# Kernel optimization log

Hardware: AMD Instinct MI355X
Metric: run time of the kernel (lower is better)

The kernel has to match this reference:

```python
import jax, jax.numpy as jnp
import numpy as np

N = 50000        # nodes
E = 1_600_000    # edges (avg degree 32)
IN = 8           # in_channels
OUT = 64         # out_channels / hidden
K = 2            # Chebyshev order


def setup_inputs() -> dict:
    key = jax.random.key(0)
    ks = jax.random.split(key, 16)
    w = lambda k, s: (jax.random.normal(k, s, jnp.float32) * 0.05)
    inp = {
        "x": jax.random.normal(ks[0], (N, IN), jnp.float32),
        "H": jax.random.normal(ks[1], (N, OUT), jnp.float32),
        "edge_index": jax.random.randint(ks[2], (2, E), 0, N, dtype=jnp.int64),
    }
    names = [("z_x", IN), ("z_h", OUT), ("r_x", IN), ("r_h", OUT), ("c_x", IN), ("c_h", OUT)]
    for i, (nm, d) in enumerate(names):
        inp["W_" + nm] = w(ks[3 + 2 * i], (K, d, OUT))
        inp["b_" + nm] = w(ks[4 + 2 * i], (OUT,))
    return inp


def _cheb(x, W, b, row, col, norm):
    # PyG-style ChebConv with lambda_max=2: L_hat = -D^{-1/2} A D^{-1/2}
    # Tx0 = x; Tx1 = L_hat x; Tx_k = 2 L_hat Tx_{k-1} - Tx_{k-2}
    out = x @ W[0]
    Tx0 = x
    Tx1 = jax.ops.segment_sum(norm[:, None] * x[col], row, num_segments=N)
    out = out + Tx1 @ W[1]
    for k in range(2, W.shape[0]):
        Tx2 = 2.0 * jax.ops.segment_sum(norm[:, None] * Tx1[col], row, num_segments=N) - Tx0
        out = out + Tx2 @ W[k]
        Tx0, Tx1 = Tx1, Tx2
    return out + b


def reference(x, H, edge_index, W_z_x, b_z_x, W_z_h, b_z_h, W_r_x, b_r_x,
              W_r_h, b_r_h, W_c_x, b_c_x, W_c_h, b_c_h):
    row, col = edge_index[0], edge_index[1]
    deg = jax.ops.segment_sum(jnp.ones((E,), x.dtype), row, num_segments=N)
    dinv = jnp.where(deg > 0, 1.0 / jnp.sqrt(jnp.where(deg > 0, deg, 1.0)), 0.0)
    norm = -dinv[row] * dinv[col]  # sym-normalized, negated adjacency (L - I)

    Z = jax.nn.sigmoid(_cheb(x, W_z_x, b_z_x, row, col, norm)
                       + _cheb(H, W_z_h, b_z_h, row, col, norm))
    R = jax.nn.sigmoid(_cheb(x, W_r_x, b_r_x, row, col, norm)
                       + _cheb(H, W_r_h, b_r_h, row, col, norm))
    C = jnp.tanh(_cheb(x, W_c_x, b_c_x, row, col, norm)
                 + _cheb(R * H, W_c_h, b_c_h, row, col, norm))
    return Z * H + (1.0 - Z) * C
```

## Files before the change

### kernel.cpp

```cpp
#include <hip/hip_runtime.h>
#include <hip/hip_fp16.h>
#include <math.h>

#define IN_CH 8
#define OUT_CH 64
#define NPW 8

__device__ __forceinline__ unsigned short f2h(float f) {
    return __half_as_ushort(__float2half_rn(f));
}
__device__ __forceinline__ float h2f_lo(unsigned v) {
    return __half2float(__ushort_as_half((unsigned short)(v & 0xFFFFu)));
}
__device__ __forceinline__ float h2f_hi(unsigned v) {
    return __half2float(__ushort_as_half((unsigned short)(v >> 16)));
}
__device__ __forceinline__ float sigmoidf(float v) { return 1.0f / (1.0f + expf(-v)); }

__global__ void deg_kernel(const int* __restrict__ row, int* __restrict__ deg, int E) {
    int i = blockIdx.x * blockDim.x + threadIdx.x;
    if (i < E) atomicAdd(&deg[row[i]], 1);
}

__global__ void dinv_kernel(const int* __restrict__ deg, float* __restrict__ dinv, int N) {
    int i = blockIdx.x * blockDim.x + threadIdx.x;
    if (i < N) {
        int d = deg[i];
        dinv[i] = (d > 0) ? rsqrtf((float)d) : 0.f;
    }
}

__global__ void scan_kernel(const int* __restrict__ deg, int* __restrict__ rowptr,
                            int* __restrict__ cursor, int N) {
    __shared__ int s_wave[17];
    __shared__ int s_running;
    int tid = threadIdx.x;
    int lane = tid & 63, wid = tid >> 6;
    if (tid == 0) s_running = 0;
    __syncthreads();
    for (int base = 0; base < N; base += 1024) {
        int i = base + tid;
        int v = (i < N) ? deg[i] : 0;
        int incl = v;
#pragma unroll
        for (int off = 1; off < 64; off <<= 1) {
            int t = __shfl_up(incl, off, 64);
            if (lane >= off) incl += t;
        }
        if (lane == 63) s_wave[wid] = incl;
        __syncthreads();
        if (wid == 0) {
            int wv = (lane < 16) ? s_wave[lane] : 0;
            int winc = wv;
#pragma unroll
            for (int off = 1; off < 16; off <<= 1) {
                int t = __shfl_up(winc, off, 64);
                if (lane >= off) winc += t;
            }
            if (lane < 16) s_wave[lane] = winc - wv;
            if (lane == 15) s_wave[16] = winc;
        }
        __syncthreads();
        int run = s_running;
        int excl = run + s_wave[wid] + incl - v;
        if (i < N) { rowptr[i] = excl; cursor[i] = excl; }
        __syncthreads();
        if (tid == 0) s_running = run + s_wave[16];
        __syncthreads();
    }
    if (tid == 0) rowptr[N] = s_running;
}

__global__ void bucket_kernel(const int* __restrict__ ei, int* __restrict__ cursor,
                              int* __restrict__ col_s, int E) {
    int e = blockIdx.x * blockDim.x + threadIdx.x;
    if (e >= E) return;
    int r = ei[e];
    int c = ei[E + e];
    int pos = atomicAdd(&cursor[r], 1);
    col_s[pos] = c;
}

__global__ void xform_kernel(const float* __restrict__ src, unsigned short* __restrict__ dst,
                             const float* __restrict__ dinv, int total4, int logd) {
    int i = blockIdx.x * blockDim.x + threadIdx.x;
    if (i >= total4) return;
    int el = i * 4;
    float s = dinv[el >> logd];
    float4 v = reinterpret_cast<const float4*>(src)[i];
    ushort4 o;
    o.x = f2h(v.x * s); o.y = f2h(v.y * s); o.z = f2h(v.z * s); o.w = f2h(v.w * s);
    reinterpret_cast<ushort4*>(dst)[i] = o;
}

__global__ void zrow_kernel(unsigned short* xb, unsigned short* Hb, unsigned short* RHb, int N) {
    int t = threadIdx.x;
    if (t < IN_CH) xb[(size_t)N * IN_CH + t] = 0;
    Hb[(size_t)N * OUT_CH + t] = 0;
    RHb[(size_t)N * OUT_CH + t] = 0;
}

__global__ void g64_kernel(const int* __restrict__ rowptr, const int* __restrict__ col_s,
                           const float* __restrict__ dinv, const unsigned short* __restrict__ srcb,
                           float* __restrict__ dst, int N) {
    int n = blockIdx.x * (blockDim.x >> 6) + (threadIdx.x >> 6);
    int lane = threadIdx.x & 63;
    int half = lane >> 5;
    int sl = lane & 31;
    if (n >= N) return;
    int beg = rowptr[n], end = rowptr[n + 1];
    const unsigned* src32 = reinterpret_cast<const unsigned*>(srcb);
    float a0 = 0.f, a1 = 0.f;
    for (int base = beg; base < end; base += 64) {
        int cnt = min(end - base, 64);
        int mycol = col_s[base + min(lane, cnt - 1)];
#pragma unroll 4
        for (int e = 0; e < cnt; e += 2) {
            int idx = e + half;
            int c = __shfl(mycol, idx, 64);
            c = (idx < cnt) ? c : N;
            unsigned v = src32[(c << 5) + sl];
            a0 += h2f_lo(v);
            a1 += h2f_hi(v);
        }
    }
    a0 += __shfl_xor(a0, 32, 64);
    a1 += __shfl_xor(a1, 32, 64);
    if (half == 0) {
        float s = -dinv[n];
        reinterpret_cast<float2*>(dst)[(size_t)n * 32 + sl] = make_float2(s * a0, s * a1);
    }
}

__global__ void g8_kernel(const int* __restrict__ rowptr, const int* __restrict__ col_s,
                          const float* __restrict__ dinv, const unsigned short* __restrict__ srcb,
                          float* __restrict__ dst, int N) {
    int n = blockIdx.x * (blockDim.x >> 6) + (threadIdx.x >> 6);
    int lane = threadIdx.x & 63;
    int g = lane >> 2;
    int o2 = lane & 3;
    if (n >= N) return;
    int beg = rowptr[n], end = rowptr[n + 1];
    const unsigned* src32 = reinterpret_cast<const unsigned*>(srcb);
    float a0 = 0.f, a1 = 0.f;
    for (int j = beg + g; j < end; j += 16) {
        int c = col_s[j];
        unsigned v = src32[(c << 2) + o2];
        a0 += h2f_lo(v);
        a1 += h2f_hi(v);
    }
#pragma unroll
    for (int m = 4; m < 64; m <<= 1) {
        a0 += __shfl_xor(a0, m, 64);
        a1 += __shfl_xor(a1, m, 64);
    }
    if (lane < 4) {
        float s = -dinv[n];
        reinterpret_cast<float2*>(dst)[(size_t)n * 4 + o2] = make_float2(s * a0, s * a1);
    }
}

__global__ __launch_bounds__(256) void gates_kernel(
        const float* __restrict__ x, const float* __restrict__ H,
        const float* __restrict__ Lx, const float* __restrict__ LH,
        const float* __restrict__ dinv,
        const float* __restrict__ Wzx, const float* __restrict__ bzx,
        const float* __restrict__ Wzh, const float* __restrict__ bzh,
        const float* __restrict__ Wrx, const float* __restrict__ brx,
        const float* __restrict__ Wrh, const float* __restrict__ brh,
        float* __restrict__ Z, float* __restrict__ RH, unsigned short* __restrict__ RHb, int N) {
    int wid = threadIdx.x >> 6;
    int lane = threadIdx.x & 63;
    int n0 = blockIdx.x * (4 * NPW) + wid * NPW;

    float axl[NPW], hreg[NPW], lhreg[NPW], accZ[NPW], accR[NPW], dv[NPW];
    float bz = bzx[lane] + bzh[lane];
    float br = brx[lane] + brh[lane];
#pragma unroll
    for (int i = 0; i < NPW; ++i) {
        int nn = min(n0 + i, N - 1);
        axl[i]   = (lane < 8) ? x[(size_t)nn * IN_CH + lane]
                 : (lane < 16 ? Lx[(size_t)nn * IN_CH + (lane - 8)] : 0.f);
        hreg[i]  = H[(size_t)nn * OUT_CH + lane];
        lhreg[i] = LH[(size_t)nn * OUT_CH + lane];
        dv[i]    = dinv[nn];
        accZ[i] = bz;
        accR[i] = br;
    }
#pragma unroll
    for (int k = 0; k < IN_CH; ++k) {
        float wz0 = Wzx[k * 64 + lane], wz1 = Wzx[512 + k * 64 + lane];
        float wr0 = Wrx[k * 64 + lane], wr1 = Wrx[512 + k * 64 + lane];
#pragma unroll
        for (int i = 0; i < NPW; ++i) {
            float xv  = __shfl(axl[i], k, 64);
            float lxv = __shfl(axl[i], k + 8, 64);
            accZ[i] = fmaf(xv, wz0, fmaf(lxv, wz1, accZ[i]));
            accR[i] = fmaf(xv, wr0, fmaf(lxv, wr1, accR[i]));
        }
    }
#pragma unroll 4
    for (int k = 0; k < OUT_CH; ++k) {
        float wh0 = Wzh[k * 64 + lane], wh1 = Wzh[4096 + k * 64 + lane];
        float wr0 = Wrh[k * 64 + lane], wr1 = Wrh[4096 + k * 64 + lane];
#pragma unroll
        for (int i = 0; i < NPW; ++i) {
            float hv  = __shfl(hreg[i], k, 64);
            float lhv = __shfl(lhreg[i], k, 64);
            accZ[i] = fmaf(hv, wh0, fmaf(lhv, wh1, accZ[i]));
            accR[i] = fmaf(hv, wr0, fmaf(lhv, wr1, accR[i]));
        }
    }
#pragma unroll
    for (int i = 0; i < NPW; ++i) {
        int n = n0 + i;
        if (n < N) {
            float z = sigmoidf(accZ[i]);
            float r = sigmoidf(accR[i]);
            float rh = r * hreg[i];
            Z[(size_t)n * OUT_CH + lane]  = z;
            RH[(size_t)n * OUT_CH + lane] = rh;
            RHb[(size_t)n * OUT_CH + lane] = f2h(dv[i] * rh);
        }
    }
}

__global__ __launch_bounds__(256) void final_kernel(
        const float* __restrict__ x, const float* __restrict__ H,
        const float* __restrict__ Lx, const float* __restrict__ RH,
        const float* __restrict__ LRH,
        const float* __restrict__ Wcx, const float* __restrict__ bcx,
        const float* __restrict__ Wch, const float* __restrict__ bch,
        const float* __restrict__ Z, float* __restrict__ out, int N) {
    int wid = threadIdx.x >> 6;
    int lane = threadIdx.x & 63;
    int n0 = blockIdx.x * (4 * NPW) + wid * NPW;

    float axl[NPW], rhreg[NPW], lrhreg[NPW], accC[NPW];
    float bc = bcx[lane] + bch[lane];
#pragma unroll
    for (int i = 0; i < NPW; ++i) {
        int nn = min(n0 + i, N - 1);
        axl[i]    = (lane < 8) ? x[(size_t)nn * IN_CH + lane]
                  : (lane < 16 ? Lx[(size_t)nn * IN_CH + (lane - 8)] : 0.f);
        rhreg[i]  = RH[(size_t)nn * OUT_CH + lane];
        lrhreg[i] = LRH[(size_t)nn * OUT_CH + lane];
        accC[i] = bc;
    }
#pragma unroll
    for (int k = 0; k < IN_CH; ++k) {
        float wc0 = Wcx[k * 64 + lane], wc1 = Wcx[512 + k * 64 + lane];
#pragma unroll
        for (int i = 0; i < NPW; ++i) {
            float xv  = __shfl(axl[i], k, 64);
            float lxv = __shfl(axl[i], k + 8, 64);
            accC[i] = fmaf(xv, wc0, fmaf(lxv, wc1, accC[i]));
        }
    }
#pragma unroll 4
    for (int k = 0; k < OUT_CH; ++k) {
        float wh0 = Wch[k * 64 + lane], wh1 = Wch[4096 + k * 64 + lane];
#pragma unroll
        for (int i = 0; i < NPW; ++i) {
            float rv  = __shfl(rhreg[i], k, 64);
            float lrv = __shfl(lrhreg[i], k, 64);
            accC[i] = fmaf(rv, wh0, fmaf(lrv, wh1, accC[i]));
        }
    }
#pragma unroll
    for (int i = 0; i < NPW; ++i) {
        int n = n0 + i;
        if (n < N) {
            float c = tanhf(accC[i]);
            float z = Z[(size_t)n * OUT_CH + lane];
            float h = H[(size_t)n * OUT_CH + lane];
            out[(size_t)n * OUT_CH + lane] = z * h + (1.0f - z) * c;
        }
    }
}

extern "C" void kernel_launch(void* const* d_in, const int* in_sizes, int n_in,
                              void* d_out, int out_size, void* d_ws, size_t ws_size,
                              hipStream_t stream) {
    const float* x   = (const float*)d_in[0];
    const float* H   = (const float*)d_in[1];
    const int*   ei  = (const int*)d_in[2];
    const float* Wzx = (const float*)d_in[3];
    const float* bzx = (const float*)d_in[4];
    const float* Wzh = (const float*)d_in[5];
    const float* bzh = (const float*)d_in[6];
    const float* Wrx = (const float*)d_in[7];
    const float* brx = (const float*)d_in[8];
    const float* Wrh = (const float*)d_in[9];
    const float* brh = (const float*)d_in[10];
    const float* Wcx = (const float*)d_in[11];
    const float* bcx = (const float*)d_in[12];
    const float* Wch = (const float*)d_in[13];
    const float* bch = (const float*)d_in[14];

    const int N = in_sizes[0] / IN_CH;
    const int E = in_sizes[2] / 2;

    int*   deg    = (int*)d_ws;
    float* dinv   = (float*)(deg + N);
    int*   rowptr = (int*)(dinv + N);
    int*   col_s  = rowptr + (N + 2);
    unsigned short* xb  = (unsigned short*)(col_s + E);
    unsigned short* Hb  = xb + (size_t)(N + 1) * IN_CH;
    unsigned short* RHb = Hb + (size_t)(N + 1) * OUT_CH;
    float* Lx  = (float*)(RHb + (size_t)(N + 1) * OUT_CH);
    float* LH  = Lx + (size_t)N * IN_CH;
    float* Z   = LH + (size_t)N * OUT_CH;
    float* RH  = Z  + (size_t)N * OUT_CH;
    float* LRH = LH;
    int*   cursor = deg;

    hipMemsetAsync(deg, 0, (size_t)N * sizeof(int), stream);

    const int tb = 256;
    deg_kernel<<<(E + tb - 1) / tb, tb, 0, stream>>>(ei, deg, E);
    dinv_kernel<<<(N + tb - 1) / tb, tb, 0, stream>>>(deg, dinv, N);
    scan_kernel<<<1, 1024, 0, stream>>>(deg, rowptr, cursor, N);
    bucket_kernel<<<(E + tb - 1) / tb, tb, 0, stream>>>(ei, cursor, col_s, E);

    {
        int t4 = N * OUT_CH / 4;
        xform_kernel<<<(t4 + tb - 1) / tb, tb, 0, stream>>>(H, Hb, dinv, t4, 6);
        t4 = N * IN_CH / 4;
        xform_kernel<<<(t4 + tb - 1) / tb, tb, 0, stream>>>(x, xb, dinv, t4, 3);
        zrow_kernel<<<1, 64, 0, stream>>>(xb, Hb, RHb, N);
    }

    const int nblk4 = (N + 3) / 4;
    const int nblkD = (N + 4 * NPW - 1) / (4 * NPW);

    g8_kernel <<<nblk4, tb, 0, stream>>>(rowptr, col_s, dinv, xb, Lx, N);
    g64_kernel<<<nblk4, tb, 0, stream>>>(rowptr, col_s, dinv, Hb, LH, N);

    gates_kernel<<<nblkD, tb, 0, stream>>>(x, H, Lx, LH, dinv, Wzx, bzx, Wzh, bzh,
                                           Wrx, brx, Wrh, brh, Z, RH, RHb, N);

    g64_kernel<<<nblk4, tb, 0, stream>>>(rowptr, col_s, dinv, RHb, LRH, N);

    final_kernel<<<nblkD, tb, 0, stream>>>(x, H, Lx, RH, LRH, Wcx, bcx, Wch, bch,
                                           Z, (float*)d_out, N);
}
```

Baseline: 661.4 us.

## Partition degree and bucket atomics by row range across block groups

Degree counting and CSR bucketing are split into 8 row-range partitions. Blocks are assigned by blockIdx mod 8, and each block scans all edges but only does atomics for rows in its own range. The intent is to localize atomic traffic (likely to an XCD/L2 slice on MI355X) so contention and cross-die coherence cost go down. In exchange, the edge row array is read 8 times.

Result: faster. 612.3 us (-7.4%).

```diff
diff --git a/kernel.cpp b/kernel.cpp
--- a/kernel.cpp
+++ b/kernel.cpp
@@ -17,9 +17,16 @@
 }
 __device__ __forceinline__ float sigmoidf(float v) { return 1.0f / (1.0f + expf(-v)); }
 
-__global__ void deg_kernel(const int* __restrict__ row, int* __restrict__ deg, int E) {
-    int i = blockIdx.x * blockDim.x + threadIdx.x;
-    if (i < E) atomicAdd(&deg[row[i]], 1);
+__global__ void degP_kernel(const int* __restrict__ row, int* __restrict__ deg,
+                            int E, int RPP) {
+    int p = blockIdx.x & 7;
+    int sub = blockIdx.x >> 3;
+    int nsub = gridDim.x >> 3;
+    int lo = p * RPP, hi = lo + RPP;
+    for (int e = sub * blockDim.x + threadIdx.x; e < E; e += nsub * blockDim.x) {
+        int r = row[e];
+        if (r >= lo && r < hi) atomicAdd(&deg[r], 1);
+    }
 }
 
 __global__ void dinv_kernel(const int* __restrict__ deg, float* __restrict__ dinv, int N) {
@@ -71,14 +78,20 @@
     if (tid == 0) rowptr[N] = s_running;
 }
 
-__global__ void bucket_kernel(const int* __restrict__ ei, int* __restrict__ cursor,
-                              int* __restrict__ col_s, int E) {
-    int e = blockIdx.x * blockDim.x + threadIdx.x;
-    if (e >= E) return;
-    int r = ei[e];
-    int c = ei[E + e];
-    int pos = atomicAdd(&cursor[r], 1);
-    col_s[pos] = c;
+__global__ void bucketP_kernel(const int* __restrict__ ei, int* __restrict__ cursor,
+                               int* __restrict__ col_s, int E, int RPP) {
+    int p = blockIdx.x & 7;
+    int sub = blockIdx.x >> 3;
+    int nsub = gridDim.x >> 3;
+    int lo = p * RPP, hi = lo + RPP;
+    for (int e = sub * blockDim.x + threadIdx.x; e < E; e += nsub * blockDim.x) {
+        int r = ei[e];
+        if (r >= lo && r < hi) {
+            int c = ei[E + e];
+            int pos = atomicAdd(&cursor[r], 1);
+            col_s[pos] = c;
+        }
+    }
 }
 
 __global__ void xform_kernel(const float* __restrict__ src, unsigned short* __restrict__ dst,
@@ -300,6 +313,7 @@
 
     const int N = in_sizes[0] / IN_CH;
     const int E = in_sizes[2] / 2;
+    const int RPP = (N + 7) / 8;
 
     int*   deg    = (int*)d_ws;
     float* dinv   = (float*)(deg + N);
@@ -318,10 +332,12 @@
     hipMemsetAsync(deg, 0, (size_t)N * sizeof(int), stream);
 
     const int tb = 256;
-    deg_kernel<<<(E + tb - 1) / tb, tb, 0, stream>>>(ei, deg, E);
+    const int nblkP = 8 * 128;
+
+    degP_kernel<<<nblkP, tb, 0, stream>>>(ei, deg, E, RPP);
     dinv_kernel<<<(N + tb - 1) / tb, tb, 0, stream>>>(deg, dinv, N);
     scan_kernel<<<1, 1024, 0, stream>>>(deg, rowptr, cursor, N);
-    bucket_kernel<<<(E + tb - 1) / tb, tb, 0, stream>>>(ei, cursor, col_s, E);
+    bucketP_kernel<<<nblkP, tb, 0, stream>>>(ei, cursor, col_s, E, RPP);
 
     {
         int t4 = N * OUT_CH / 4;
```
